# Kernel tuning notes

Hardware: AMD Instinct MI355X
Metric: run time of the kernel (lower is better)

The kernel has to match this reference:

```python
import jax, jax.numpy as jnp
import numpy as np

B, H, LB, PW, TC = 4096, 64, 32, 16, 1
WL = LB + PW  # window_length = look_back + prediction


def setup_inputs() -> dict:
    key = jax.random.key(0)
    ks = jax.random.split(key, 9)
    bnd = 1.0 / np.sqrt(H)  # torch Linear default init bound
    bnd_h = 1.0 / np.sqrt(H)
    return {
        "x": jax.random.normal(ks[0], (B, LB, TC), jnp.float32),
        "F_w": jax.random.uniform(ks[1], (WL, H, H), jnp.float32, -bnd, bnd),
        "F_b": jax.random.uniform(ks[2], (WL, H), jnp.float32, -bnd, bnd),
        "H_w": jax.random.uniform(ks[3], (WL, TC, H), jnp.float32, -bnd_h, bnd_h),
        "H_b": jax.random.uniform(ks[4], (WL, TC), jnp.float32, -bnd_h, bnd_h),
        "initial_state": jax.random.normal(ks[5], (H,), jnp.float32),
        "initial_covariance": 0.1 * jax.random.normal(ks[6], (H, H), jnp.float32),
        "Q": 0.1 * jax.random.normal(ks[7], (H, H), jnp.float32),
        "R": jnp.eye(TC, dtype=jnp.float32) + 0.1 * jax.random.normal(ks[8], (TC, TC), jnp.float32),
    }


def _kalman_forward(x, F_w, F_b, H_w, H_b, s0, P0, Q, R):
    nb = x.shape[0]
    hs = jnp.broadcast_to(s0, (nb, H))          # (B,H)
    P = jnp.broadcast_to(P0, (nb, H, H))        # (B,H,H)
    ys = jnp.moveaxis(x[:, :LB, :TC], 0, 1)     # (LB,B,TC) per-step observations

    @jax.checkpoint
    def kf_step(carry, inp):
        hs, P = carry
        Fw, Fb, Hw, Hb, y = inp
        hs_pred = hs @ Fw.T + Fb                                        # (B,H)
        P_pred = jnp.einsum('ij,bjk,lk->bil', Fw, P, Fw) + Q            # F P F^T + Q
        resid = y - (hs_pred @ Hw.T + Hb)                               # (B,TC)
        S = jnp.einsum('ij,bjk,lk->bil', Hw, P_pred, Hw) + R            # (B,TC,TC)
        K = jnp.einsum('bij,kj->bik', P_pred, Hw) @ jnp.linalg.inv(S)   # (B,H,TC)
        hs_new = hs_pred + jnp.einsum('bij,bj->bi', K, resid)
        P_new = P_pred - jnp.einsum('bit,tj,bjk->bik', K, Hw, P_pred)   # (I-KH)P_pred
        return (hs_new, P_new), None

    (hs, _), _ = jax.lax.scan(
        kf_step, (hs, P), (F_w[:LB], F_b[:LB], H_w[:LB], H_b[:LB], ys))

    def pred_step(hs, inp):
        Fw, Fb, Hw, Hb = inp
        hs = hs @ Fw.T + Fb
        return hs, hs @ Hw.T + Hb

    _, ems = jax.lax.scan(
        pred_step, hs, (F_w[LB:], F_b[LB:], H_w[LB:], H_b[LB:]))  # (PW,B,TC)
    # torch.cat(preds, dim=1).unsqueeze(-1) -> (B, PW*TC, 1)
    return jnp.moveaxis(ems, 0, 1).reshape(nb, PW * TC)[..., None]


def reference(x, F_w, F_b, H_w, H_b, initial_state, initial_covariance, Q, R):
    return _kalman_forward(x, F_w, F_b, H_w, H_b, initial_state, initial_covariance, Q, R)
```

## Files before the change

kernel.cpp:

```cpp
#include <hip/hip_runtime.h>


constexpr int KP_OFF = 0;
constexpr int WP_OFF = 2048;
constexpr int UP_OFF = 4160;
constexpr int EP_OFF = 5184;
constexpr int CNT_OFF = 5200;
constexpr int WS_U64 = 5201;

typedef float    f32x4 __attribute__((ext_vector_type(4)));
typedef _Float16 f16x4 __attribute__((ext_vector_type(4)));

#define MFMA16(a, b, c) __builtin_amdgcn_mfma_f32_16x16x16f16((a), (b), (c), 0, 0, 0)

template <int CTRL>
__device__ __forceinline__ float dpp_add(float x) {
  int v = __builtin_amdgcn_update_dpp(0, __builtin_bit_cast(int, x), CTRL, 0xf, 0xf, true);
  return x + __builtin_bit_cast(float, v);
}
__device__ __forceinline__ float sum16(float x) {
  x = dpp_add<0xB1>(x);
  x = dpp_add<0x4E>(x);
  x = dpp_add<0x141>(x);
  x = dpp_add<0x140>(x);
  return x;
}
__device__ __forceinline__ float xrow_sum(float x) {
  const float a = __shfl_xor(x, 16, 64);
  const float b = __shfl_xor(x, 32, 64);
  const float c = __shfl_xor(x, 48, 64);
  return (x + a) + (b + c);
}

__device__ __forceinline__ float spin_read(const unsigned long long* p, unsigned tag) {
  unsigned long long v = 0;
  for (int it = 0; it < (1 << 22); ++it) {
    v = __hip_atomic_load(p, __ATOMIC_RELAXED, __HIP_MEMORY_SCOPE_AGENT);
    if ((unsigned)(v >> 32) == tag) break;
  }
  union { unsigned u; float f; } cv; cv.u = (unsigned)v;
  return cv.f;
}
__device__ __forceinline__ float spin_read_sleep(const unsigned long long* p, unsigned tag) {
  unsigned long long v = 0;
  for (int it = 0; it < (1 << 20); ++it) {
    v = __hip_atomic_load(p, __ATOMIC_RELAXED, __HIP_MEMORY_SCOPE_AGENT);
    if ((unsigned)(v >> 32) == tag) break;
    __builtin_amdgcn_s_sleep(2);
  }
  union { unsigned u; float f; } cv; cv.u = (unsigned)v;
  return cv.f;
}
__device__ __forceinline__ void pub_write(unsigned long long* p, unsigned tag, float x) {
  union { float f; unsigned u; } cv; cv.f = x;
  __hip_atomic_store(p, ((unsigned long long)tag << 32) | cv.u,
                     __ATOMIC_RELAXED, __HIP_MEMORY_SCOPE_AGENT);
}
__device__ __forceinline__ void lds_barrier() {
  asm volatile("s_waitcnt lgkmcnt(0)" ::: "memory");
  __builtin_amdgcn_sched_barrier(0);
  __builtin_amdgcn_s_barrier();
  __builtin_amdgcn_sched_barrier(0);
}

__global__ __launch_bounds__(256, 1) void kalman_fused(
    const float* __restrict__ Fw, const float* __restrict__ Fb,
    const float* __restrict__ Hw, const float* __restrict__ Hb,
    const float* __restrict__ s0, const float* __restrict__ P0,
    const float* __restrict__ Qg, const float* __restrict__ Rg,
    const float* __restrict__ x, float* __restrict__ out,
    unsigned long long* __restrict__ ws) {
  __shared__ __align__(16) char smem[58368];
  const int tid  = threadIdx.x;
  const int lane = tid & 63;
  const int w    = tid >> 6;
  const int blk  = blockIdx.x;
  unsigned long long* kp = ws + KP_OFF;
  unsigned long long* wp = ws + WP_OFF;
  unsigned long long* up = ws + UP_OFF;
  unsigned long long* ep = ws + EP_OFF;

  if (blk == 0) {
    float*    QL = (float*)smem;
    float*    HL = (float*)(smem + 16384);
    _Float16* FF = (_Float16*)(smem + 24576);
    float*    kL = (float*)(smem + 57344);
    const int l15 = lane & 15, g = lane >> 4;

    for (int slot = tid; slot < 1024; slot += 256) {
      const int f = slot >> 6, ln = slot & 63;
      const int a = f >> 2, b = f & 3, g2 = ln >> 4, l2 = ln & 15;
      f32x4 v;
      #pragma unroll
      for (int r = 0; r < 4; ++r)
        v[r] = Qg[(16 * a + 4 * g2 + r) * 64 + 16 * b + l2];
      *(f32x4*)&QL[slot * 4] = v;
    }
    for (int idx = tid; idx < 2048; idx += 256) HL[idx] = Hw[idx];
    for (int s = tid; s < 2048; s += 256) {
      const int mat = s >> 10, s2 = s & 1023;
      const int r = s2 >> 4, c4 = (s2 & 15) * 4;
      const f32x4 v = *(const f32x4*)(Fw + mat * 4096 + r * 64 + c4);
      f16x4 hf;
      #pragma unroll
      for (int j = 0; j < 4; ++j) hf[j] = (_Float16)v[j];
      const int tile = (r >> 4) * 4 + (c4 >> 4);
      const int ln = (r & 15) + 16 * ((c4 & 15) >> 2);
      *(f16x4*)&FF[((mat * 16 + tile) * 64 + ln) * 4] = hf;
    }
    __syncthreads();

    if (w != 0) {
      for (int c = 0; c < 16; ++c) {
        if (c < 15) {
          const float* Fbase = Fw + (size_t)(2 * c + 2) * 4096;
          _Float16* dstbuf = FF + (((c + 1) & 1) * 2 * 16) * 64 * 4;
          for (int s = (w - 1) * 64 + lane; s < 2048; s += 192) {
            const int mat = s >> 10, s2 = s & 1023;
            const int r = s2 >> 4, c4 = (s2 & 15) * 4;
            const f32x4 v = *(const f32x4*)(Fbase + mat * 4096 + r * 64 + c4);
            f16x4 hf;
            #pragma unroll
            for (int j = 0; j < 4; ++j) hf[j] = (_Float16)v[j];
            const int tile = (r >> 4) * 4 + (c4 >> 4);
            const int ln = (r & 15) + 16 * ((c4 & 15) >> 2);
            *(f16x4*)&dstbuf[((mat * 16 + tile) * 64 + ln) * 4] = hf;
          }
        }
        lds_barrier();
        if (w == 1) {
          #pragma unroll
          for (int mm = 0; mm < 2; ++mm) {
            const int t = 2 * c - 1 + mm;
            if (t >= 0 && t <= 30)
              pub_write(&kp[t * 64 + lane], (unsigned)(t + 1), kL[(t & 3) * 64 + lane]);
          }
        }
      }
      return;
    }

    const float R0 = Rg[0];
    f32x4 PF[4][4];
    #pragma unroll
    for (int a = 0; a < 4; ++a)
      #pragma unroll
      for (int b = 0; b < 4; ++b)
        #pragma unroll
        for (int r = 0; r < 4; ++r)
          PF[a][b][r] = P0[(16 * a + 4 * g + r) * 64 + 16 * b + l15];

    f32x4 numf[4];
    float hpc[4] = {0.f, 0.f, 0.f, 0.f};
    float Sv = 0.f;
    #pragma unroll
    for (int a = 0; a < 4; ++a) numf[a] = (f32x4){0.f, 0.f, 0.f, 0.f};

    for (int c = 0; c < 16; ++c) {
      #pragma unroll
      for (int m = 0; m < 2; ++m) {
        const int t = 2 * c + m;
        f16x4 Fh[4][4];
        {
          const _Float16* src = FF + (((c & 1) * 2 + m) * 16) * 64 * 4;
          #pragma unroll
          for (int a = 0; a < 4; ++a)
            #pragma unroll
            for (int b = 0; b < 4; ++b)
              Fh[a][b] = *(const f16x4*)&src[((a * 4 + b) * 64 + lane) * 4];
        }
        f32x4 hrow[4];
        float hcol[4];
        #pragma unroll
        for (int a = 0; a < 4; ++a)
          hrow[a] = *(const f32x4*)&HL[t * 64 + 16 * a + 4 * g];
        #pragma unroll
        for (int b = 0; b < 4; ++b) hcol[b] = HL[t * 64 + 16 * b + l15];

        const float rcpS = 1.0f / (Sv + R0);
        f32x4 krow[4];
        #pragma unroll
        for (int a = 0; a < 4; ++a) krow[a] = numf[a] * rcpS;
        if (t > 0 && l15 == 0) {
          #pragma unroll
          for (int a = 0; a < 4; ++a)
            *(f32x4*)&kL[((t - 1) & 3) * 64 + 16 * a + 4 * g] = krow[a];
        }
        f16x4 Uh[4][4];
        #pragma unroll
        for (int ti = 0; ti < 4; ++ti) {
          f16x4 Ah[4], Al[4];
          #pragma unroll
          for (int kc = 0; kc < 4; ++kc) {
            const f32x4 p = PF[kc][ti] - krow[kc] * hpc[ti];
            #pragma unroll
            for (int j = 0; j < 4; ++j) {
              const _Float16 h_ = (_Float16)p[j];
              Ah[kc][j] = h_;
              Al[kc][j] = (_Float16)((p[j] - (float)h_) * 2048.0f);
            }
          }
          #pragma unroll
          for (int tj = 0; tj < 4; ++tj) {
            f32x4 am = {0.f, 0.f, 0.f, 0.f}, a2 = {0.f, 0.f, 0.f, 0.f};
            #pragma unroll
            for (int kc = 0; kc < 4; ++kc) {
              am = MFMA16(Ah[kc], Fh[tj][kc], am);
              a2 = MFMA16(Al[kc], Fh[tj][kc], a2);
            }
            const f32x4 u = am + a2 * (1.0f / 2048.0f);
            f16x4 uh;
            #pragma unroll
            for (int j = 0; j < 4; ++j) uh[j] = (_Float16)u[j];
            Uh[ti][tj] = uh;
          }
        }
        #pragma unroll
        for (int ti = 0; ti < 4; ++ti)
          #pragma unroll
          for (int tj = 0; tj < 4; ++tj) {
            f32x4 acc = *(const f32x4*)&QL[((ti * 4 + tj) * 64 + lane) * 4];
            #pragma unroll
            for (int kc = 0; kc < 4; ++kc)
              acc = MFMA16(Uh[kc][ti], Fh[tj][kc], acc);
            PF[ti][tj] = acc;
          }
        #pragma unroll
        for (int a = 0; a < 4; ++a) {
          f32x4 np = PF[a][0] * hcol[0] + PF[a][1] * hcol[1] +
                     PF[a][2] * hcol[2] + PF[a][3] * hcol[3];
          #pragma unroll
          for (int r = 0; r < 4; ++r) np[r] = sum16(np[r]);
          numf[a] = np;
        }
        #pragma unroll
        for (int b = 0; b < 4; ++b) {
          float hp = 0.f;
          #pragma unroll
          for (int a = 0; a < 4; ++a) {
            const f32x4 tv = hrow[a] * PF[a][b];
            hp += (tv.x + tv.y) + (tv.z + tv.w);
          }
          hpc[b] = xrow_sum(hp);
        }
        {
          float sp = 0.f;
          #pragma unroll
          for (int a = 0; a < 4; ++a) {
            const f32x4 tv = hrow[a] * numf[a];
            sp += (tv.x + tv.y) + (tv.z + tv.w);
          }
          Sv = xrow_sum(sp);
        }
      }
      lds_barrier();
    }
    {
      const float rcpS = 1.0f / (Sv + R0);
      if (l15 == 0) {
        #pragma unroll
        for (int a = 0; a < 4; ++a)
          *(f32x4*)&kL[3 * 64 + 16 * a + 4 * g] = numf[a] * rcpS;
      }
      asm volatile("s_waitcnt lgkmcnt(0)" ::: "memory");
      pub_write(&kp[31 * 64 + lane], 32u, kL[3 * 64 + lane]);
    }
    return;
  }

  if (blk == 1) {
    const int plist[4] = {w, 7 - w, 8 + w, 15 - w};
    #pragma unroll
    for (int pi = 0; pi < 4; ++pi) {
      const int p = plist[pi];
      const int q = 32 + p;
      float r = Hw[q * 64 + lane];
      float eacc = 0.f;
      for (int s = 0; s <= p; ++s) {
        const int m = q - s;
        eacc += r * Fb[m * 64 + lane];
        const float* Fm = Fw + (size_t)m * 4096;
        float r0 = 0.f, r1 = 0.f, r2 = 0.f, r3 = 0.f;
        for (int j = 0; j < 64; j += 4) {
          r0 += __shfl(r, j,     64) * Fm[j * 64 + lane];
          r1 += __shfl(r, j + 1, 64) * Fm[(j + 1) * 64 + lane];
          r2 += __shfl(r, j + 2, 64) * Fm[(j + 2) * 64 + lane];
          r3 += __shfl(r, j + 3, 64) * Fm[(j + 3) * 64 + lane];
        }
        r = (r0 + r1) + (r2 + r3);
      }
      eacc = xrow_sum(sum16(eacc));
      pub_write(&up[p * 64 + lane], 1u, r);
      if (lane == 0) pub_write(&ep[p], 1u, eacc + Hb[q]);
    }
    __syncthreads();
    if (tid == 0)
      __hip_atomic_fetch_add(&ws[CNT_OFF], 1ull, __ATOMIC_RELAXED, __HIP_MEMORY_SCOPE_AGENT);
    return;
  }

  if (blk < 11) {
    float* vb = (float*)smem + w * 64;
    const int c = (blk - 2) * 4 + w;
    if (c > 32) return;
    if (c == 32) {
      pub_write(&wp[32 * 64 + lane], 1u, spin_read_sleep(&kp[31 * 64 + lane], 32u));
      if (lane == 0)
        __hip_atomic_fetch_add(&ws[CNT_OFF], 1ull, __ATOMIC_RELAXED, __HIP_MEMORY_SCOPE_AGENT);
      return;
    }
    const int t0 = (c == 0) ? 0 : c;
    float v = (c == 0) ? s0[lane] : spin_read_sleep(&kp[(c - 1) * 64 + lane], (unsigned)c);
    f32x4 fn[16];
    {
      const float* Fr = Fw + (size_t)t0 * 4096 + lane * 64;
      #pragma unroll
      for (int jc = 0; jc < 16; ++jc) fn[jc] = *(const f32x4*)(Fr + jc * 4);
    }
    float hn  = Hw[t0 * 64 + lane];
    float fbn = (c == 0) ? Fb[t0 * 64 + lane] : 0.f;
    for (int t = t0; t < 32; ++t) {
      vb[lane] = v;
      f32x4 fc[16];
      #pragma unroll
      for (int jc = 0; jc < 16; ++jc) fc[jc] = fn[jc];
      const float ht = hn, fbt = fbn;
      if (t + 1 < 32) {
        const float* Fr = Fw + (size_t)(t + 1) * 4096 + lane * 64;
        #pragma unroll
        for (int jc = 0; jc < 16; ++jc) fn[jc] = *(const f32x4*)(Fr + jc * 4);
        hn = Hw[(t + 1) * 64 + lane];
        if (c == 0) fbn = Fb[(t + 1) * 64 + lane];
      }
      float a0 = fbt, a1 = 0.f, a2 = 0.f, a3 = 0.f;
      #pragma unroll
      for (int jc = 0; jc < 16; ++jc) {
        const f32x4 vv = *(const f32x4*)(vb + jc * 4);
        a0 += fc[jc].x * vv.x; a1 += fc[jc].y * vv.y;
        a2 += fc[jc].z * vv.z; a3 += fc[jc].w * vv.w;
      }
      const float vp = (a0 + a1) + (a2 + a3);
      float hv = xrow_sum(sum16(ht * vp));
      if (c == 0) hv += Hb[t];
      const float kt = spin_read_sleep(&kp[t * 64 + lane], (unsigned)(t + 1));
      v = vp - kt * hv;
    }
    pub_write(&wp[c * 64 + lane], 1u, v);
    if (lane == 0)
      __hip_atomic_fetch_add(&ws[CNT_OFF], 1ull, __ATOMIC_RELAXED, __HIP_MEMORY_SCOPE_AGENT);
    return;
  }

  {
    float* Ul = (float*)smem;
    float* Wl = (float*)(smem + 4352);
    float* Zl = (float*)(smem + 13328);
    float* El = (float*)(smem + 15504);
    const int b = (blk - 11) * 256 + tid;
    f32x4 xr[8];
    const f32x4* xp = (const f32x4*)(x + (size_t)b * 32);
    #pragma unroll
    for (int u = 0; u < 8; ++u) xr[u] = xp[u];

    if (tid == 0) {
      for (int it = 0; it < (1 << 20); ++it) {
        if (__hip_atomic_load(&ws[CNT_OFF], __ATOMIC_RELAXED, __HIP_MEMORY_SCOPE_AGENT) >= 34ull)
          break;
        __builtin_amdgcn_s_sleep(8);
      }
    }
    __syncthreads();
    for (int idx = tid; idx < 1024; idx += 256)
      Ul[(idx >> 6) * 68 + (idx & 63)] = spin_read(&up[idx], 1u);
    for (int idx = tid; idx < 2112; idx += 256)
      Wl[(idx >> 6) * 68 + (idx & 63)] = spin_read(&wp[idx], 1u);
    if (tid < 16) El[tid] = spin_read(&ep[tid], 1u);
    __syncthreads();
    for (int idx = tid; idx < 528; idx += 256) {
      const int p = idx / 33, cc = idx - p * 33;
      const float* Up = Ul + p * 68;
      const float* Wc = Wl + cc * 68;
      float a0 = 0.f, a1 = 0.f, a2 = 0.f, a3 = 0.f;
      #pragma unroll 4
      for (int i = 0; i < 64; i += 4) {
        a0 += Up[i] * Wc[i];         a1 += Up[i + 1] * Wc[i + 1];
        a2 += Up[i + 2] * Wc[i + 2]; a3 += Up[i + 3] * Wc[i + 3];
      }
      float z = (a0 + a1) + (a2 + a3);
      if (cc == 0) z += El[p];
      Zl[p * 34 + cc] = z;
    }
    __syncthreads();
    float acc[16];
    #pragma unroll
    for (int p = 0; p < 16; ++p) acc[p] = Zl[p * 34];
    #pragma unroll
    for (int u = 0; u < 8; ++u) {
      #pragma unroll
      for (int e = 0; e < 4; ++e) {
        const float xval = xr[u][e];
        const int t = u * 4 + e;
        #pragma unroll
        for (int p = 0; p < 16; ++p) acc[p] += Zl[p * 34 + 1 + t] * xval;
      }
    }
    float4* op = (float4*)(out + (size_t)b * 16);
    op[0] = make_float4(acc[0], acc[1], acc[2], acc[3]);
    op[1] = make_float4(acc[4], acc[5], acc[6], acc[7]);
    op[2] = make_float4(acc[8], acc[9], acc[10], acc[11]);
    op[3] = make_float4(acc[12], acc[13], acc[14], acc[15]);
  }
}

extern "C" void kernel_launch(void* const* d_in, const int* in_sizes, int n_in,
                              void* d_out, int out_size, void* d_ws, size_t ws_size,
                              hipStream_t stream) {
  (void)in_sizes; (void)n_in; (void)out_size; (void)ws_size;
  const float* x  = (const float*)d_in[0];
  const float* Fw = (const float*)d_in[1];
  const float* Fb = (const float*)d_in[2];
  const float* Hw = (const float*)d_in[3];
  const float* Hb = (const float*)d_in[4];
  const float* s0 = (const float*)d_in[5];
  const float* P0 = (const float*)d_in[6];
  const float* Q  = (const float*)d_in[7];
  const float* R  = (const float*)d_in[8];
  float* out = (float*)d_out;
  unsigned long long* ws = (unsigned long long*)d_ws;

  hipMemsetAsync(d_ws, 0, WS_U64 * sizeof(unsigned long long), stream);
  kalman_fused<<<27, 256, 0, stream>>>(Fw, Fb, Hw, Hb, s0, P0, Q, R, x, out, ws);
}
```

Before: 127.1 us.

## Move gain-propagation chains into block 0 using MFMA with LDS-shared Kalman gains

```diff
diff --git a/kernel.cpp b/kernel.cpp
--- a/kernel.cpp
+++ b/kernel.cpp
@@ -1,7 +1,6 @@
 #include <hip/hip_runtime.h>
 
 
-constexpr int KP_OFF = 0;
 constexpr int WP_OFF = 2048;
 constexpr int UP_OFF = 4160;
 constexpr int EP_OFF = 5184;
@@ -37,16 +36,6 @@
   for (int it = 0; it < (1 << 22); ++it) {
     v = __hip_atomic_load(p, __ATOMIC_RELAXED, __HIP_MEMORY_SCOPE_AGENT);
     if ((unsigned)(v >> 32) == tag) break;
-  }
-  union { unsigned u; float f; } cv; cv.u = (unsigned)v;
-  return cv.f;
-}
-__device__ __forceinline__ float spin_read_sleep(const unsigned long long* p, unsigned tag) {
-  unsigned long long v = 0;
-  for (int it = 0; it < (1 << 20); ++it) {
-    v = __hip_atomic_load(p, __ATOMIC_RELAXED, __HIP_MEMORY_SCOPE_AGENT);
-    if ((unsigned)(v >> 32) == tag) break;
-    __builtin_amdgcn_s_sleep(2);
   }
   union { unsigned u; float f; } cv; cv.u = (unsigned)v;
   return cv.f;
@@ -75,16 +64,16 @@
   const int lane = tid & 63;
   const int w    = tid >> 6;
   const int blk  = blockIdx.x;
-  unsigned long long* kp = ws + KP_OFF;
   unsigned long long* wp = ws + WP_OFF;
   unsigned long long* up = ws + UP_OFF;
   unsigned long long* ep = ws + EP_OFF;
 
   if (blk == 0) {
-    float*    QL = (float*)smem;
-    float*    HL = (float*)(smem + 16384);
-    _Float16* FF = (_Float16*)(smem + 24576);
-    float*    kL = (float*)(smem + 57344);
+    float*    QL  = (float*)smem;
+    _Float16* FHI = (_Float16*)(smem + 16384);
+    _Float16* FLO = (_Float16*)(smem + 32768);
+    _Float16* UL  = (_Float16*)(smem + 49152);
+    float*    kL  = (float*)(smem + 57344);
     const int l15 = lane & 15, g = lane >> 4;
 
     for (int slot = tid; slot < 1024; slot += 256) {
@@ -96,108 +85,82 @@
         v[r] = Qg[(16 * a + 4 * g2 + r) * 64 + 16 * b + l2];
       *(f32x4*)&QL[slot * 4] = v;
     }
-    for (int idx = tid; idx < 2048; idx += 256) HL[idx] = Hw[idx];
-    for (int s = tid; s < 2048; s += 256) {
-      const int mat = s >> 10, s2 = s & 1023;
-      const int r = s2 >> 4, c4 = (s2 & 15) * 4;
-      const f32x4 v = *(const f32x4*)(Fw + mat * 4096 + r * 64 + c4);
-      f16x4 hf;
-      #pragma unroll
-      for (int j = 0; j < 4; ++j) hf[j] = (_Float16)v[j];
+    for (int s = tid; s < 1024; s += 256) {
+      const int r = s >> 4, c4 = (s & 15) * 4;
+      const f32x4 v = *(const f32x4*)(Fw + r * 64 + c4);
+      f16x4 hi, lo;
+      #pragma unroll
+      for (int j = 0; j < 4; ++j) {
+        const _Float16 h_ = (_Float16)v[j];
+        hi[j] = h_;
+        lo[j] = (_Float16)((v[j] - (float)h_) * 2048.0f);
+      }
       const int tile = (r >> 4) * 4 + (c4 >> 4);
       const int ln = (r & 15) + 16 * ((c4 & 15) >> 2);
-      *(f16x4*)&FF[((mat * 16 + tile) * 64 + ln) * 4] = hf;
-    }
-    __syncthreads();
-
-    if (w != 0) {
-      for (int c = 0; c < 16; ++c) {
-        if (c < 15) {
-          const float* Fbase = Fw + (size_t)(2 * c + 2) * 4096;
-          _Float16* dstbuf = FF + (((c + 1) & 1) * 2 * 16) * 64 * 4;
-          for (int s = (w - 1) * 64 + lane; s < 2048; s += 192) {
-            const int mat = s >> 10, s2 = s & 1023;
-            const int r = s2 >> 4, c4 = (s2 & 15) * 4;
-            const f32x4 v = *(const f32x4*)(Fbase + mat * 4096 + r * 64 + c4);
-            f16x4 hf;
-            #pragma unroll
-            for (int j = 0; j < 4; ++j) hf[j] = (_Float16)v[j];
+      *(f16x4*)&FHI[(tile * 64 + ln) * 4] = hi;
+      *(f16x4*)&FLO[(tile * 64 + ln) * 4] = lo;
+    }
+    __syncthreads();
+
+    if (w == 3) {
+      for (int t = 0; t < 32; ++t) {
+        if (t + 1 < 32) {
+          const float* Fbase = Fw + (size_t)(t + 1) * 4096;
+          _Float16* dh = FHI + ((t + 1) & 1) * 4096;
+          _Float16* dl = FLO + ((t + 1) & 1) * 4096;
+          #pragma unroll
+          for (int it = 0; it < 16; ++it) {
+            const int s = lane + it * 64;
+            const int r = s >> 4, c4 = (s & 15) * 4;
+            const f32x4 v = *(const f32x4*)(Fbase + r * 64 + c4);
+            f16x4 hi, lo;
+            #pragma unroll
+            for (int j = 0; j < 4; ++j) {
+              const _Float16 h_ = (_Float16)v[j];
+              hi[j] = h_;
+              lo[j] = (_Float16)((v[j] - (float)h_) * 2048.0f);
+            }
             const int tile = (r >> 4) * 4 + (c4 >> 4);
             const int ln = (r & 15) + 16 * ((c4 & 15) >> 2);
-            *(f16x4*)&dstbuf[((mat * 16 + tile) * 64 + ln) * 4] = hf;
+            *(f16x4*)&dh[(tile * 64 + ln) * 4] = hi;
+            *(f16x4*)&dl[(tile * 64 + ln) * 4] = lo;
           }
         }
         lds_barrier();
-        if (w == 1) {
-          #pragma unroll
-          for (int mm = 0; mm < 2; ++mm) {
-            const int t = 2 * c - 1 + mm;
-            if (t >= 0 && t <= 30)
-              pub_write(&kp[t * 64 + lane], (unsigned)(t + 1), kL[(t & 3) * 64 + lane]);
-          }
-        }
-      }
-      return;
-    }
-
-    const float R0 = Rg[0];
-    f32x4 PF[4][4];
-    #pragma unroll
-    for (int a = 0; a < 4; ++a)
-      #pragma unroll
-      for (int b = 0; b < 4; ++b)
-        #pragma unroll
-        for (int r = 0; r < 4; ++r)
-          PF[a][b][r] = P0[(16 * a + 4 * g + r) * 64 + 16 * b + l15];
-
-    f32x4 numf[4];
-    float hpc[4] = {0.f, 0.f, 0.f, 0.f};
-    float Sv = 0.f;
-    #pragma unroll
-    for (int a = 0; a < 4; ++a) numf[a] = (f32x4){0.f, 0.f, 0.f, 0.f};
-
-    for (int c = 0; c < 16; ++c) {
-      #pragma unroll
-      for (int m = 0; m < 2; ++m) {
-        const int t = 2 * c + m;
-        f16x4 Fh[4][4];
-        {
-          const _Float16* src = FF + (((c & 1) * 2 + m) * 16) * 64 * 4;
-          #pragma unroll
-          for (int a = 0; a < 4; ++a)
-            #pragma unroll
-            for (int b = 0; b < 4; ++b)
-              Fh[a][b] = *(const f16x4*)&src[((a * 4 + b) * 64 + lane) * 4];
-        }
-        f32x4 hrow[4];
-        float hcol[4];
-        #pragma unroll
-        for (int a = 0; a < 4; ++a)
-          hrow[a] = *(const f32x4*)&HL[t * 64 + 16 * a + 4 * g];
-        #pragma unroll
-        for (int b = 0; b < 4; ++b) hcol[b] = HL[t * 64 + 16 * b + l15];
-
-        const float rcpS = 1.0f / (Sv + R0);
-        f32x4 krow[4];
-        #pragma unroll
-        for (int a = 0; a < 4; ++a) krow[a] = numf[a] * rcpS;
-        if (t > 0 && l15 == 0) {
-          #pragma unroll
-          for (int a = 0; a < 4; ++a)
-            *(f32x4*)&kL[((t - 1) & 3) * 64 + 16 * a + 4 * g] = krow[a];
-        }
-        f16x4 Uh[4][4];
+      }
+      pub_write(&wp[32 * 64 + lane], 1u, kL[3 * 64 + lane]);
+    } else if (w == 0) {
+      const float R0 = Rg[0];
+      f32x4 PF[4][4];
+      #pragma unroll
+      for (int a = 0; a < 4; ++a)
+        #pragma unroll
+        for (int b = 0; b < 4; ++b)
+          #pragma unroll
+          for (int r = 0; r < 4; ++r)
+            PF[a][b][r] = P0[(16 * a + 4 * g + r) * 64 + 16 * b + l15];
+      f32x4 krow[4];
+      float hpc[4] = {0.f, 0.f, 0.f, 0.f};
+      #pragma unroll
+      for (int a = 0; a < 4; ++a) krow[a] = (f32x4){0.f, 0.f, 0.f, 0.f};
+
+      for (int t = 0; t < 32; ++t) {
+        const _Float16* fh = FHI + (t & 1) * 4096;
+        f16x4 Fh0[4];
+        #pragma unroll
+        for (int kc = 0; kc < 4; ++kc)
+          Fh0[kc] = *(const f16x4*)&fh[(kc * 64 + lane) * 4];
         #pragma unroll
         for (int ti = 0; ti < 4; ++ti) {
           f16x4 Ah[4], Al[4];
           #pragma unroll
           for (int kc = 0; kc < 4; ++kc) {
-            const f32x4 p = PF[kc][ti] - krow[kc] * hpc[ti];
+            const f32x4 p4 = PF[kc][ti] - krow[kc] * hpc[ti];
             #pragma unroll
             for (int j = 0; j < 4; ++j) {
-              const _Float16 h_ = (_Float16)p[j];
+              const _Float16 h_ = (_Float16)p4[j];
               Ah[kc][j] = h_;
-              Al[kc][j] = (_Float16)((p[j] - (float)h_) * 2048.0f);
+              Al[kc][j] = (_Float16)((p4[j] - (float)h_) * 2048.0f);
             }
           }
           #pragma unroll
@@ -205,26 +168,46 @@
             f32x4 am = {0.f, 0.f, 0.f, 0.f}, a2 = {0.f, 0.f, 0.f, 0.f};
             #pragma unroll
             for (int kc = 0; kc < 4; ++kc) {
-              am = MFMA16(Ah[kc], Fh[tj][kc], am);
-              a2 = MFMA16(Al[kc], Fh[tj][kc], a2);
+              const f16x4 bh = (tj == 0) ? Fh0[kc]
+                  : *(const f16x4*)&fh[((tj * 4 + kc) * 64 + lane) * 4];
+              am = MFMA16(Ah[kc], bh, am);
+              a2 = MFMA16(Al[kc], bh, a2);
             }
             const f32x4 u = am + a2 * (1.0f / 2048.0f);
             f16x4 uh;
             #pragma unroll
             for (int j = 0; j < 4; ++j) uh[j] = (_Float16)u[j];
-            Uh[ti][tj] = uh;
-          }
-        }
-        #pragma unroll
-        for (int ti = 0; ti < 4; ++ti)
+            *(f16x4*)&UL[((ti * 4 + tj) * 64 + lane) * 4] = uh;
+          }
+        }
+        asm volatile("s_waitcnt lgkmcnt(0)" ::: "memory");
+        __builtin_amdgcn_sched_barrier(0);
+        f32x4 hrow[4];
+        float hcol[4];
+        #pragma unroll
+        for (int a = 0; a < 4; ++a)
+          hrow[a] = *(const f32x4*)(Hw + t * 64 + 16 * a + 4 * g);
+        #pragma unroll
+        for (int b = 0; b < 4; ++b) hcol[b] = Hw[t * 64 + 16 * b + l15];
+        #pragma unroll
+        for (int ti = 0; ti < 4; ++ti) {
+          f16x4 Ua[4];
+          #pragma unroll
+          for (int kc = 0; kc < 4; ++kc)
+            Ua[kc] = *(const f16x4*)&UL[((kc * 4 + ti) * 64 + lane) * 4];
           #pragma unroll
           for (int tj = 0; tj < 4; ++tj) {
             f32x4 acc = *(const f32x4*)&QL[((ti * 4 + tj) * 64 + lane) * 4];
             #pragma unroll
-            for (int kc = 0; kc < 4; ++kc)
-              acc = MFMA16(Uh[kc][ti], Fh[tj][kc], acc);
+            for (int kc = 0; kc < 4; ++kc) {
+              const f16x4 bh = (tj == 0) ? Fh0[kc]
+                  : *(const f16x4*)&fh[((tj * 4 + kc) * 64 + lane) * 4];
+              acc = MFMA16(Ua[kc], bh, acc);
+            }
             PF[ti][tj] = acc;
           }
+        }
+        f32x4 numf[4];
         #pragma unroll
         for (int a = 0; a < 4; ++a) {
           f32x4 np = PF[a][0] * hcol[0] + PF[a][1] * hcol[1] +
@@ -243,55 +226,98 @@
           }
           hpc[b] = xrow_sum(hp);
         }
-        {
-          float sp = 0.f;
-          #pragma unroll
-          for (int a = 0; a < 4; ++a) {
-            const f32x4 tv = hrow[a] * numf[a];
-            sp += (tv.x + tv.y) + (tv.z + tv.w);
-          }
-          Sv = xrow_sum(sp);
-        }
-      }
-      lds_barrier();
-    }
-    {
-      const float rcpS = 1.0f / (Sv + R0);
-      if (l15 == 0) {
-        #pragma unroll
-        for (int a = 0; a < 4; ++a)
-          *(f32x4*)&kL[3 * 64 + 16 * a + 4 * g] = numf[a] * rcpS;
-      }
-      asm volatile("s_waitcnt lgkmcnt(0)" ::: "memory");
-      pub_write(&kp[31 * 64 + lane], 32u, kL[3 * 64 + lane]);
-    }
-    return;
-  }
-
-  if (blk == 1) {
-    const int plist[4] = {w, 7 - w, 8 + w, 15 - w};
-    #pragma unroll
-    for (int pi = 0; pi < 4; ++pi) {
-      const int p = plist[pi];
-      const int q = 32 + p;
-      float r = Hw[q * 64 + lane];
-      float eacc = 0.f;
-      for (int s = 0; s <= p; ++s) {
-        const int m = q - s;
-        eacc += r * Fb[m * 64 + lane];
-        const float* Fm = Fw + (size_t)m * 4096;
-        float r0 = 0.f, r1 = 0.f, r2 = 0.f, r3 = 0.f;
-        for (int j = 0; j < 64; j += 4) {
-          r0 += __shfl(r, j,     64) * Fm[j * 64 + lane];
-          r1 += __shfl(r, j + 1, 64) * Fm[(j + 1) * 64 + lane];
-          r2 += __shfl(r, j + 2, 64) * Fm[(j + 2) * 64 + lane];
-          r3 += __shfl(r, j + 3, 64) * Fm[(j + 3) * 64 + lane];
-        }
-        r = (r0 + r1) + (r2 + r3);
-      }
-      eacc = xrow_sum(sum16(eacc));
-      pub_write(&up[p * 64 + lane], 1u, r);
-      if (lane == 0) pub_write(&ep[p], 1u, eacc + Hb[q]);
+        float sp = 0.f;
+        #pragma unroll
+        for (int a = 0; a < 4; ++a) {
+          const f32x4 tv = hrow[a] * numf[a];
+          sp += (tv.x + tv.y) + (tv.z + tv.w);
+        }
+        const float Sv = xrow_sum(sp);
+        const float rcpS = 1.0f / (Sv + R0);
+        #pragma unroll
+        for (int a = 0; a < 4; ++a) krow[a] = numf[a] * rcpS;
+        if (l15 == 0) {
+          #pragma unroll
+          for (int a = 0; a < 4; ++a)
+            *(f32x4*)&kL[(t & 3) * 64 + 16 * a + 4 * g] = krow[a];
+        }
+        lds_barrier();
+      }
+    } else {
+      const int ct = w - 1;
+      f16x4 VbH[4], VbL[4];
+      #pragma unroll
+      for (int kc = 0; kc < 4; ++kc) {
+        const f32x4 s4 = *(const f32x4*)(s0 + 16 * kc + 4 * g);
+        #pragma unroll
+        for (int j = 0; j < 4; ++j) {
+          const float v = (ct == 0 && l15 == 0) ? s4[j] : 0.f;
+          const _Float16 h_ = (_Float16)v;
+          VbH[kc][j] = h_;
+          VbL[kc][j] = (_Float16)((v - (float)h_) * 2048.0f);
+        }
+      }
+      f32x4 vpv[4];
+      float qreg = 0.f;
+      for (int t = 0; t < 32; ++t) {
+        if (t > 0) {
+          #pragma unroll
+          for (int rt = 0; rt < 4; ++rt) {
+            const f32x4 k4 = *(const f32x4*)&kL[((t - 1) & 3) * 64 + 16 * rt + 4 * g];
+            #pragma unroll
+            for (int j = 0; j < 4; ++j) {
+              float val = vpv[rt][j] - k4[j] * qreg;
+              if (l15 == t - 16 * ct) val = k4[j];
+              const _Float16 h_ = (_Float16)val;
+              VbH[rt][j] = h_;
+              VbL[rt][j] = (_Float16)((val - (float)h_) * 2048.0f);
+            }
+          }
+        }
+        const _Float16* fh = FHI + (t & 1) * 4096;
+        const _Float16* fl = FLO + (t & 1) * 4096;
+        #pragma unroll
+        for (int rt = 0; rt < 4; ++rt) {
+          f32x4 am, a1;
+          if (ct == 0 && l15 == 0) {
+            const f32x4 fb4 = *(const f32x4*)(Fb + t * 64 + 16 * rt + 4 * g);
+            am = fb4;
+          } else {
+            am = (f32x4){0.f, 0.f, 0.f, 0.f};
+          }
+          a1 = (f32x4){0.f, 0.f, 0.f, 0.f};
+          #pragma unroll
+          for (int kc = 0; kc < 4; ++kc) {
+            const f16x4 ah = *(const f16x4*)&fh[((rt * 4 + kc) * 64 + lane) * 4];
+            const f16x4 al = *(const f16x4*)&fl[((rt * 4 + kc) * 64 + lane) * 4];
+            am = MFMA16(ah, VbH[kc], am);
+            a1 = MFMA16(ah, VbL[kc], a1);
+            a1 = MFMA16(al, VbH[kc], a1);
+          }
+          vpv[rt] = am + a1 * (1.0f / 2048.0f);
+        }
+        float qp = 0.f;
+        #pragma unroll
+        for (int rt = 0; rt < 4; ++rt) {
+          const f32x4 h4 = *(const f32x4*)(Hw + t * 64 + 16 * rt + 4 * g);
+          qp += h4.x * vpv[rt].x + h4.y * vpv[rt].y +
+                h4.z * vpv[rt].z + h4.w * vpv[rt].w;
+        }
+        qp += __shfl_xor(qp, 16, 64);
+        qp += __shfl_xor(qp, 32, 64);
+        if (ct == 0 && l15 == 0) qp += Hb[t];
+        qreg = qp;
+        lds_barrier();
+      }
+      #pragma unroll
+      for (int rt = 0; rt < 4; ++rt) {
+        const f32x4 k4 = *(const f32x4*)&kL[3 * 64 + 16 * rt + 4 * g];
+        #pragma unroll
+        for (int j = 0; j < 4; ++j) {
+          const float val = vpv[rt][j] - k4[j] * qreg;
+          pub_write(&wp[(16 * ct + l15) * 64 + 16 * rt + 4 * g + j], 1u, val);
+        }
+      }
     }
     __syncthreads();
     if (tid == 0)
@@ -299,54 +325,29 @@
     return;
   }
 
-  if (blk < 11) {
-    float* vb = (float*)smem + w * 64;
-    const int c = (blk - 2) * 4 + w;
-    if (c > 32) return;
-    if (c == 32) {
-      pub_write(&wp[32 * 64 + lane], 1u, spin_read_sleep(&kp[31 * 64 + lane], 32u));
-      if (lane == 0)
-        __hip_atomic_fetch_add(&ws[CNT_OFF], 1ull, __ATOMIC_RELAXED, __HIP_MEMORY_SCOPE_AGENT);
-      return;
-    }
-    const int t0 = (c == 0) ? 0 : c;
-    float v = (c == 0) ? s0[lane] : spin_read_sleep(&kp[(c - 1) * 64 + lane], (unsigned)c);
-    f32x4 fn[16];
-    {
-      const float* Fr = Fw + (size_t)t0 * 4096 + lane * 64;
-      #pragma unroll
-      for (int jc = 0; jc < 16; ++jc) fn[jc] = *(const f32x4*)(Fr + jc * 4);
-    }
-    float hn  = Hw[t0 * 64 + lane];
-    float fbn = (c == 0) ? Fb[t0 * 64 + lane] : 0.f;
-    for (int t = t0; t < 32; ++t) {
-      vb[lane] = v;
-      f32x4 fc[16];
-      #pragma unroll
-      for (int jc = 0; jc < 16; ++jc) fc[jc] = fn[jc];
-      const float ht = hn, fbt = fbn;
-      if (t + 1 < 32) {
-        const float* Fr = Fw + (size_t)(t + 1) * 4096 + lane * 64;
-        #pragma unroll
-        for (int jc = 0; jc < 16; ++jc) fn[jc] = *(const f32x4*)(Fr + jc * 4);
-        hn = Hw[(t + 1) * 64 + lane];
-        if (c == 0) fbn = Fb[(t + 1) * 64 + lane];
-      }
-      float a0 = fbt, a1 = 0.f, a2 = 0.f, a3 = 0.f;
-      #pragma unroll
-      for (int jc = 0; jc < 16; ++jc) {
-        const f32x4 vv = *(const f32x4*)(vb + jc * 4);
-        a0 += fc[jc].x * vv.x; a1 += fc[jc].y * vv.y;
-        a2 += fc[jc].z * vv.z; a3 += fc[jc].w * vv.w;
-      }
-      const float vp = (a0 + a1) + (a2 + a3);
-      float hv = xrow_sum(sum16(ht * vp));
-      if (c == 0) hv += Hb[t];
-      const float kt = spin_read_sleep(&kp[t * 64 + lane], (unsigned)(t + 1));
-      v = vp - kt * hv;
-    }
-    pub_write(&wp[c * 64 + lane], 1u, v);
-    if (lane == 0)
+  if (blk <= 4) {
+    const int p = (blk - 1) * 4 + w;
+    const int q = 32 + p;
+    float r = Hw[q * 64 + lane];
+    float eacc = 0.f;
+    for (int s = 0; s <= p; ++s) {
+      const int m = q - s;
+      eacc += r * Fb[m * 64 + lane];
+      const float* Fm = Fw + (size_t)m * 4096;
+      float r0 = 0.f, r1 = 0.f, r2 = 0.f, r3 = 0.f;
+      for (int j = 0; j < 64; j += 4) {
+        r0 += __shfl(r, j,     64) * Fm[j * 64 + lane];
+        r1 += __shfl(r, j + 1, 64) * Fm[(j + 1) * 64 + lane];
+        r2 += __shfl(r, j + 2, 64) * Fm[(j + 2) * 64 + lane];
+        r3 += __shfl(r, j + 3, 64) * Fm[(j + 3) * 64 + lane];
+      }
+      r = (r0 + r1) + (r2 + r3);
+    }
+    eacc = xrow_sum(sum16(eacc));
+    pub_write(&up[p * 64 + lane], 1u, r);
+    if (lane == 0) pub_write(&ep[p], 1u, eacc + Hb[q]);
+    __syncthreads();
+    if (tid == 0)
       __hip_atomic_fetch_add(&ws[CNT_OFF], 1ull, __ATOMIC_RELAXED, __HIP_MEMORY_SCOPE_AGENT);
     return;
   }
@@ -356,15 +357,15 @@
     float* Wl = (float*)(smem + 4352);
     float* Zl = (float*)(smem + 13328);
     float* El = (float*)(smem + 15504);
-    const int b = (blk - 11) * 256 + tid;
+    const int b = (blk - 5) * 256 + tid;
     f32x4 xr[8];
     const f32x4* xp = (const f32x4*)(x + (size_t)b * 32);
     #pragma unroll
     for (int u = 0; u < 8; ++u) xr[u] = xp[u];
 
     if (tid == 0) {
-      for (int it = 0; it < (1 << 20); ++it) {
-        if (__hip_atomic_load(&ws[CNT_OFF], __ATOMIC_RELAXED, __HIP_MEMORY_SCOPE_AGENT) >= 34ull)
+      for (int it = 0; it < (1 << 22); ++it) {
+        if (__hip_atomic_load(&ws[CNT_OFF], __ATOMIC_RELAXED, __HIP_MEMORY_SCOPE_AGENT) >= 5ull)
           break;
         __builtin_amdgcn_s_sleep(8);
       }
@@ -429,5 +430,5 @@
   unsigned long long* ws = (unsigned long long*)d_ws;
 
   hipMemsetAsync(d_ws, 0, WS_U64 * sizeof(unsigned long long), stream);
-  kalman_fused<<<27, 256, 0, stream>>>(Fw, Fb, Hw, Hb, s0, P0, Q, R, x, out, ws);
-}
+  kalman_fused<<<21, 256, 0, stream>>>(Fw, Fb, Hw, Hb, s0, P0, Q, R, x, out, ws);
+}
```

Result: slower. 156.9 us (+23.4%).
